# Kernel optimization log

Measured on AMD Instinct MI355X. Metric: run time of the kernel, lower is better.

Reference implementation:

```python
import jax, jax.numpy as jnp
import numpy as np

V, E, H = 2048, 512, 1024  # vocab, emb_dim, hid_dim
B, L = 128, 256            # batch, seq_len


def _gru_cell(x, h, W_ih, W_hh, b_ih, b_hh):
    # PyTorch GRU cell math. x: [B, in], h: [B, H]
    gi = x @ W_ih.T + b_ih            # [B, 3H]
    gh = h @ W_hh.T + b_hh            # [B, 3H]
    i_r, i_z, i_n = jnp.split(gi, 3, axis=-1)
    h_r, h_z, h_n = jnp.split(gh, 3, axis=-1)
    r = jax.nn.sigmoid(i_r + h_r)
    z = jax.nn.sigmoid(i_z + h_z)
    n = jnp.tanh(i_n + r * h_n)
    return (1.0 - z) * n + z * h


def setup_inputs() -> dict:
    key = jax.random.key(0)
    ks = jax.random.split(key, 16)
    s = 0.05
    emb_enc = jax.random.normal(ks[0], (V, E), jnp.float32) * s
    emb_dec = jax.random.normal(ks[1], (V, E), jnp.float32) * s
    # padding_idx=0 rows are zero in nn.Embedding
    emb_enc = emb_enc.at[0].set(0.0)
    emb_dec = emb_dec.at[0].set(0.0)
    inp = {
        "seq": jax.random.randint(ks[2], (B, L), 0, V, jnp.int64 if jax.config.jax_enable_x64 else jnp.int32),
        "teacher_forcing_ratio": 1,
        "emb_enc": emb_enc,
        "W_ih_e": jax.random.normal(ks[3], (3 * H, E), jnp.float32) * s,
        "W_hh_e": jax.random.normal(ks[4], (3 * H, H), jnp.float32) * s,
        "b_ih_e": jax.random.normal(ks[5], (3 * H,), jnp.float32) * s,
        "b_hh_e": jax.random.normal(ks[6], (3 * H,), jnp.float32) * s,
        "emb_dec": emb_dec,
        "W_ih_d": jax.random.normal(ks[7], (3 * H, E + H), jnp.float32) * s,
        "W_hh_d": jax.random.normal(ks[8], (3 * H, H), jnp.float32) * s,
        "b_ih_d": jax.random.normal(ks[9], (3 * H,), jnp.float32) * s,
        "b_hh_d": jax.random.normal(ks[10], (3 * H,), jnp.float32) * s,
        "fc_W": jax.random.normal(ks[11], (V, E + 2 * H), jnp.float32) * s,
        "fc_b": jax.random.normal(ks[12], (V,), jnp.float32) * s,
    }
    return inp


def reference(seq, teacher_forcing_ratio, emb_enc, W_ih_e, W_hh_e, b_ih_e, b_hh_e,
              emb_dec, W_ih_d, W_hh_d, b_ih_d, b_hh_d, fc_W, fc_b):
    # ---- Encoder: GRU over embedded seq (dropout_p=0, eval mode) ----
    x_emb = emb_enc[seq]                       # [B, L, E]
    h0 = jnp.zeros((seq.shape[0], H), x_emb.dtype)

    def enc_step(h, x_t):
        return _gru_cell(x_t, h, W_ih_e, W_hh_e, b_ih_e, b_hh_e), None

    context, _ = jax.lax.scan(enc_step, h0, jnp.swapaxes(x_emb, 0, 1))  # [B, H]
    mu = jnp.zeros((seq.shape[0], H), jnp.float32)
    log_var = jnp.zeros((seq.shape[0], H), jnp.float32)

    # ---- Decoder: teacher_forcing_ratio=1 -> inputs are seq[:, t-1] for step t ----
    dec_in = emb_dec[seq[:, :-1]]              # [B, L-1, E]

    def dec_step(h, e_t):
        x = jnp.concatenate([e_t, context], axis=-1)            # [B, E+H]
        h2 = _gru_cell(x, h, W_ih_d, W_hh_d, b_ih_d, b_hh_d)    # [B, H]
        feat = jnp.concatenate([e_t, h2, context], axis=-1)     # [B, E+2H]
        pred = feat @ fc_W.T + fc_b                             # [B, V]
        return h2, pred

    _, preds = jax.lax.scan(dec_step, context, jnp.swapaxes(dec_in, 0, 1))  # [L-1, B, V]
    preds = jnp.swapaxes(preds, 0, 1)                                        # [B, L-1, V]
    outputs = jnp.concatenate(
        [jnp.zeros((seq.shape[0], 1, V), preds.dtype), preds], axis=1)      # [B, L, V]
    return outputs, context, mu, log_var
```

## Files before the change

### kernel.cpp

```cpp
#include <hip/hip_runtime.h>
#include <math.h>

#define KV 2048
#define KE 512
#define KH 1024
#define KB 128
#define KL 256
#define KH3 3072
#define TCH 32
#define NSLOT 33

typedef __attribute__((ext_vector_type(8))) short s8v;
typedef __attribute__((ext_vector_type(8))) unsigned short u16x8;
typedef __attribute__((ext_vector_type(4))) float f4v;

__device__ __forceinline__ unsigned short f2b(float f) {
    unsigned u = __float_as_uint(f);
    u += 0x7fffu + ((u >> 16) & 1u);
    return (unsigned short)(u >> 16);
}
__device__ __forceinline__ float b2f(unsigned short h) {
    return __uint_as_float(((unsigned)h) << 16);
}

template<int ROWS>
__device__ __forceinline__ void stage_tile(unsigned short* lds,
                                           const unsigned short* g, int ld)
{
    const int tid = threadIdx.x;
    const int wave = tid >> 6, lane = tid & 63;
    constexpr int per_wave = ROWS / 32;
    #pragma unroll
    for (int i = 0; i < per_wave; ++i) {
        const int r0 = (wave * per_wave + i) * 8;
        const int r  = r0 + (lane >> 3);
        const int cg = (lane & 7) ^ (r & 7);
        const unsigned short* gp = g + (size_t)r * ld + cg * 8;
        __builtin_amdgcn_global_load_lds(
            (const __attribute__((address_space(1))) unsigned int*)(const void*)gp,
            (__attribute__((address_space(3))) unsigned int*)(void*)(lds + r0 * 64),
            16, 0, 0);
    }
}

__global__ __launch_bounds__(256)
void gemm128(const unsigned short* __restrict__ A, int lda,
             const unsigned short* __restrict__ Bm, int ldb,
             float* __restrict__ OutF, unsigned short* __restrict__ OutH,
             int N, int K,
             const float* __restrict__ bias,
             const float* __restrict__ addrow,
             int scatter, int t0)
{
    __shared__ unsigned short As[128 * 64];
    __shared__ unsigned short Bs[128 * 64];
    const int tid = threadIdx.x;
    const int wave = tid >> 6, lane = tid & 63;
    const int wm = wave >> 1, wn = wave & 1;
    const int q = lane >> 4, l15 = lane & 15, l7 = lane & 7;
    const int m0 = blockIdx.y * 128, n0 = blockIdx.x * 128;
    f4v acc[4][4] = {};
    for (int kb = 0; kb < K; kb += 64) {
        stage_tile<128>(As, A + (size_t)m0 * lda + kb, lda);
        stage_tile<128>(Bs, Bm + (size_t)n0 * ldb + kb, ldb);
        __syncthreads();
        #pragma unroll
        for (int kk = 0; kk < 2; ++kk) {
            const int ch = (kk * 4 + q) ^ l7;
            s8v a[4], b[4];
            #pragma unroll
            for (int i = 0; i < 4; ++i) {
                a[i] = *(const s8v*)(As + (wm * 64 + i * 16 + l15) * 64 + ch * 8);
                b[i] = *(const s8v*)(Bs + (wn * 64 + i * 16 + l15) * 64 + ch * 8);
            }
            #pragma unroll
            for (int i = 0; i < 4; ++i)
                #pragma unroll
                for (int j = 0; j < 4; ++j)
                    acc[i][j] = __builtin_amdgcn_mfma_f32_16x16x32_bf16(
                        a[i], b[j], acc[i][j], 0, 0, 0);
        }
        __syncthreads();
    }
    #pragma unroll
    for (int i = 0; i < 4; ++i) {
        #pragma unroll
        for (int r = 0; r < 4; ++r) {
            const int row = m0 + wm * 64 + i * 16 + q * 4 + r;
            size_t obase;
            if (scatter) {
                const int bidx = row & 127, tl = row >> 7;
                obase = (size_t)(bidx * KL + t0 + tl + 1) * KV;
            } else {
                obase = (size_t)row * N;
            }
            #pragma unroll
            for (int j = 0; j < 4; ++j) {
                const int col = n0 + wn * 64 + j * 16 + l15;
                float v = acc[i][j][r];
                if (bias)   v += bias[col];
                if (addrow) v += addrow[(size_t)(row & 127) * N + col];
                if (OutF) OutF[obase + col] = v;
                else      OutH[obase + col] = f2b(v);
            }
        }
    }
}

__global__ __launch_bounds__(256)
void rec_fused(const unsigned short* __restrict__ gi,
               const float* __restrict__ ci,
               unsigned short* hbring,
               float* __restrict__ h,
               unsigned short* __restrict__ h2,
               const unsigned short* __restrict__ Whh,
               const float* __restrict__ bhh,
               unsigned* bar, int Tc, unsigned gen0, int slot0)
{
    __shared__ unsigned short Ws[3 * 16 * KH];
    __shared__ float Pp[4 * 6 * 4 * 16 * 4];
    __shared__ unsigned short Hs[32 * 16];
    unsigned* flags = bar + 64;
    const int tid  = threadIdx.x;
    const int wave = tid >> 6, lane = tid & 63;
    const int q = lane >> 4, l15 = lane & 15;
    const int mg  = (int)blockIdx.x & 3;
    const int m0  = mg * 32;
    const int hc0 = ((int)blockIdx.x >> 2) * 16;

    #pragma unroll
    for (int it = 0; it < 24; ++it) {
        const int gidx = it * 256 + tid;
        const int row  = gidx >> 7;
        const int slot = gidx & 127;
        const int csrc = slot ^ (row & 7);
        const int g = row >> 4, rr = row & 15;
        const unsigned short* src =
            Whh + (size_t)(g * KH + hc0 + rr) * KH + csrc * 8;
        __builtin_amdgcn_global_load_lds(
            (const __attribute__((address_space(1))) unsigned int*)(const void*)src,
            (__attribute__((address_space(3))) unsigned int*)(void*)(Ws + row * KH + slot * 8),
            16, 0, 0);
    }

    const int col16 = tid & 15;
    const int rowq  = (tid >> 4) & 15;
    const int qq = rowq >> 2, r4 = rowq & 3;
    const int col = hc0 + col16;
    float bh[3], civ[2][3], hv[2];
    #pragma unroll
    for (int g = 0; g < 3; ++g) bh[g] = bhh[g * KH + col];
    #pragma unroll
    for (int i = 0; i < 2; ++i) {
        const int row = m0 + i * 16 + rowq;
        hv[i] = h[(size_t)row * KH + col];
        #pragma unroll
        for (int g = 0; g < 3; ++g)
            civ[i][g] = ci ? ci[(size_t)row * KH3 + g * KH + col] : 0.0f;
    }
    __syncthreads();

    const unsigned* fp = flags + mg * 64 + lane;

    for (int tl = 0; tl < Tc; ++tl) {
        int sl = slot0 + tl;       if (sl >= NSLOT) sl -= NSLOT;
        int slw = sl + 1;          if (slw >= NSLOT) slw -= NSLOT;
        const unsigned short* hin  = hbring + (size_t)sl  * KB * KH;
        unsigned short*       hout = hbring + (size_t)slw * KB * KH;

        float gir[2][3];
        #pragma unroll
        for (int i = 0; i < 2; ++i) {
            const size_t gib = ((size_t)tl * KB + m0 + i * 16 + rowq) * KH3 + col;
            gir[i][0] = b2f(gi[gib]);
            gir[i][1] = b2f(gi[gib + KH]);
            gir[i][2] = b2f(gi[gib + 2 * KH]);
        }

        if (tl > 0) {
            const unsigned tgt = gen0 + (unsigned)tl;
            while (true) {
                unsigned v;
                asm volatile("global_load_dword %0, %1, off sc0 sc1\n\t"
                             "s_waitcnt vmcnt(0)"
                             : "=v"(v) : "v"(fp) : "memory");
                if (!__any((int)(v < tgt))) break;
                __builtin_amdgcn_s_sleep(1);
            }
        }

        s8v a[2][8];
        #pragma unroll
        for (int i = 0; i < 2; ++i)
            #pragma unroll
            for (int kk = 0; kk < 8; ++kk)
                a[i][kk] = *(const s8v*)(hin +
                    (size_t)(m0 + i * 16 + l15) * KH + wave * 256 + kk * 32 + q * 8);

        f4v acc[2][3] = {};
        #pragma unroll
        for (int kk = 0; kk < 8; ++kk) {
            const int soff = ((wave * 32 + kk * 4 + q) ^ (l15 & 7)) * 8;
            #pragma unroll
            for (int g = 0; g < 3; ++g) {
                const s8v bf = *(const s8v*)(Ws + (g * 16 + l15) * KH + soff);
                acc[0][g] = __builtin_amdgcn_mfma_f32_16x16x32_bf16(
                    a[0][kk], bf, acc[0][g], 0, 0, 0);
                acc[1][g] = __builtin_amdgcn_mfma_f32_16x16x32_bf16(
                    a[1][kk], bf, acc[1][g], 0, 0, 0);
            }
        }
        #pragma unroll
        for (int i = 0; i < 2; ++i)
            #pragma unroll
            for (int g = 0; g < 3; ++g)
                *(f4v*)(Pp + (((wave * 6 + i * 3 + g) * 4 + q) * 16 + l15) * 4)
                    = acc[i][g];
        __syncthreads();
        #pragma unroll
        for (int i = 0; i < 2; ++i) {
            float gs0 = 0.f, gs1 = 0.f, gs2 = 0.f;
            #pragma unroll
            for (int w = 0; w < 4; ++w) {
                const float* p = Pp + ((w * 6 + i * 3) * 4 + qq) * 64
                               + col16 * 4 + r4;
                gs0 += p[0]; gs1 += p[256]; gs2 += p[512];
            }
            const float rg = 1.0f / (1.0f + __expf(-(gir[i][0] + civ[i][0] + gs0 + bh[0])));
            const float zg = 1.0f / (1.0f + __expf(-(gir[i][1] + civ[i][1] + gs1 + bh[1])));
            const float ng = tanhf(gir[i][2] + civ[i][2] + rg * (gs2 + bh[2]));
            hv[i] = (1.0f - zg) * ng + zg * hv[i];
            const unsigned short hb16 = f2b(hv[i]);
            const int li = i * 16 + rowq;
            Hs[li * 16 + col16] = hb16;
            if (h2) h2[((size_t)tl * KB + m0 + li) * (KE + KH) + col] = hb16;
        }
        __syncthreads();
        if (wave == 0) {
            const int row = lane >> 1, half = lane & 1;
            const u16x8 hval = *(const u16x8*)(Hs + row * 16 + half * 8);
            const unsigned short* sp =
                hout + (size_t)(m0 + row) * KH + hc0 + half * 8;
            asm volatile("global_store_dwordx4 %0, %1, off sc0 sc1"
                         :: "v"(sp), "v"(hval) : "memory");
            asm volatile("s_waitcnt vmcnt(0)" ::: "memory");
            if (lane == 0) {
                const unsigned tgt = gen0 + (unsigned)tl + 1u;
                const unsigned* fpw = flags + mg * 64 + ((int)blockIdx.x >> 2);
                asm volatile("global_store_dword %0, %1, off sc0 sc1"
                             :: "v"(fpw), "v"(tgt) : "memory");
            }
        }
    }
    #pragma unroll
    for (int i = 0; i < 2; ++i)
        h[(size_t)(m0 + i * 16 + rowq) * KH + col] = hv[i];
}

static void launch_rec(const unsigned short* gi, const float* ci,
                       unsigned short* hbring, float* h, unsigned short* h2,
                       const unsigned short* Whh, const float* bhh,
                       unsigned* bar, int Tc, unsigned gen0, int slot0,
                       hipStream_t stream)
{
    void* args[11] = { (void*)&gi, (void*)&ci, (void*)&hbring, (void*)&h,
                       (void*)&h2, (void*)&Whh, (void*)&bhh, (void*)&bar,
                       (void*)&Tc, (void*)&gen0, (void*)&slot0 };
    hipLaunchCooperativeKernel((const void*)rec_fused, dim3(256), dim3(256),
                               args, 0, stream);
}

__global__ __launch_bounds__(256)
void gather_emb(const float* __restrict__ emb, const int* __restrict__ seq,
                unsigned short* __restrict__ X, int ldx, int t0)
{
    const int idx = blockIdx.x * 256 + threadIdx.x;
    const int e8 = idx & 63;
    const int rr = idx >> 6;
    const int b = rr & 127, tl = rr >> 7;
    const int tok = seq[b * KL + t0 + tl];
    const float4* src = (const float4*)(emb + (size_t)tok * KE + e8 * 8);
    const float4 v0 = src[0], v1 = src[1];
    u16x8 o;
    o[0] = f2b(v0.x); o[1] = f2b(v0.y); o[2] = f2b(v0.z); o[3] = f2b(v0.w);
    o[4] = f2b(v1.x); o[5] = f2b(v1.y); o[6] = f2b(v1.z); o[7] = f2b(v1.w);
    *(u16x8*)(X + (size_t)rr * ldx + e8 * 8) = o;
}

__global__ __launch_bounds__(256)
void f32tobf16(const float* __restrict__ src, unsigned short* __restrict__ dst, int n)
{
    const int i = (blockIdx.x * 256 + threadIdx.x) * 4;
    if (i < n) {
        const float4 v = *(const float4*)(src + i);
        dst[i] = f2b(v.x); dst[i + 1] = f2b(v.y);
        dst[i + 2] = f2b(v.z); dst[i + 3] = f2b(v.w);
    }
}

__global__ __launch_bounds__(256)
void zero_f32(float* __restrict__ p, int n)
{
    const int i = blockIdx.x * 256 + threadIdx.x;
    if (i < n) p[i] = 0.0f;
}

__global__ __launch_bounds__(256)
void zero_u16(unsigned short* __restrict__ p, int n)
{
    const int i = blockIdx.x * 256 + threadIdx.x;
    if (i < n) p[i] = 0;
}

__global__ __launch_bounds__(256)
void copy_f32(float* __restrict__ dst, const float* __restrict__ src, int n)
{
    const int i = blockIdx.x * 256 + threadIdx.x;
    if (i < n) dst[i] = src[i];
}

__global__ __launch_bounds__(256)
void zero_row0(float* __restrict__ out)
{
    const int idx = blockIdx.x * 256 + threadIdx.x;
    const int b = idx >> 11, v = idx & (KV - 1);
    out[(size_t)b * KL * KV + v] = 0.0f;
}

extern "C" void kernel_launch(void* const* d_in, const int* in_sizes, int n_in,
                              void* d_out, int out_size, void* d_ws, size_t ws_size,
                              hipStream_t stream)
{
    (void)in_sizes; (void)n_in; (void)out_size; (void)ws_size;
    const int*   seq     = (const int*)  d_in[0];
    const float* emb_enc = (const float*)d_in[2];
    const float* W_ih_e  = (const float*)d_in[3];
    const float* W_hh_e  = (const float*)d_in[4];
    const float* b_ih_e  = (const float*)d_in[5];
    const float* b_hh_e  = (const float*)d_in[6];
    const float* emb_dec = (const float*)d_in[7];
    const float* W_ih_d  = (const float*)d_in[8];
    const float* W_hh_d  = (const float*)d_in[9];
    const float* b_ih_d  = (const float*)d_in[10];
    const float* b_hh_d  = (const float*)d_in[11];
    const float* fc_W    = (const float*)d_in[12];
    const float* fc_b    = (const float*)d_in[13];
    float* out = (float*)d_out;

    char* w = (char*)d_ws;
    unsigned*       bar     = (unsigned*)w;                  w += 2048;
    unsigned short* Wb_ih_e = (unsigned short*)w;            w += (size_t)KH3 * KE * 2;
    unsigned short* Wb_hh_e = (unsigned short*)w;            w += (size_t)KH3 * KH * 2;
    unsigned short* Wb_ih_d = (unsigned short*)w;            w += (size_t)KH3 * (KE + KH) * 2;
    unsigned short* Wb_hh_d = (unsigned short*)w;            w += (size_t)KH3 * KH * 2;
    unsigned short* fc_Wb   = (unsigned short*)w;            w += (size_t)KV * (KE + 2 * KH) * 2;
    float*          h       = (float*)w;                     w += (size_t)KB * KH * 4;
    unsigned short* hbring  = (unsigned short*)w;            w += (size_t)NSLOT * KB * KH * 2;
    float*          ci      = (float*)w;                     w += (size_t)KB * KH3 * 4;
    float*          cf      = (float*)w;                     w += (size_t)KB * KV * 4;
    unsigned short* gi      = (unsigned short*)w;            w += (size_t)TCH * KB * KH3 * 2;
    unsigned short* featc   = (unsigned short*)w;            w += (size_t)TCH * KB * (KE + KH) * 2;

    f32tobf16<<<(KH3 * KE) / 1024, 256, 0, stream>>>(W_ih_e, Wb_ih_e, KH3 * KE);
    f32tobf16<<<(KH3 * KH) / 1024, 256, 0, stream>>>(W_hh_e, Wb_hh_e, KH3 * KH);
    f32tobf16<<<(KH3 * (KE + KH)) / 1024, 256, 0, stream>>>(W_ih_d, Wb_ih_d, KH3 * (KE + KH));
    f32tobf16<<<(KH3 * KH) / 1024, 256, 0, stream>>>(W_hh_d, Wb_hh_d, KH3 * KH);
    f32tobf16<<<(KV * (KE + 2 * KH)) / 1024, 256, 0, stream>>>(fc_W, fc_Wb, KV * (KE + 2 * KH));

    zero_f32<<<2, 256, 0, stream>>>((float*)bar, 512);
    zero_f32<<<(KB * KH) / 256, 256, 0, stream>>>(h, KB * KH);
    zero_u16<<<(KB * KH) / 256, 256, 0, stream>>>(hbring, KB * KH);

    unsigned gen0 = 0;
    int slot = 0;

    for (int t0 = 0; t0 < KL; t0 += TCH) {
        unsigned short* Xc = featc;
        gather_emb<<<(TCH * KB * 64) / 256, 256, 0, stream>>>(emb_enc, seq, Xc, KE, t0);
        gemm128<<<dim3(KH3 / 128, (TCH * KB) / 128), 256, 0, stream>>>(
            Xc, KE, Wb_ih_e, KE, nullptr, gi, KH3, KE, b_ih_e, nullptr, 0, 0);
        launch_rec(gi, nullptr, hbring, h, nullptr, Wb_hh_e, b_hh_e, bar,
                   TCH, gen0, slot, stream);
        gen0 += TCH;
        slot = (slot + TCH) % NSLOT;
    }

    const unsigned short* ctxb = hbring + (size_t)slot * KB * KH;

    float* ctx_out = out + (size_t)KB * KL * KV;
    copy_f32<<<(KB * KH) / 256, 256, 0, stream>>>(ctx_out, h, KB * KH);
    zero_f32<<<(2 * KB * KH) / 256, 256, 0, stream>>>(ctx_out + KB * KH, 2 * KB * KH);
    zero_row0<<<(KB * KV) / 256, 256, 0, stream>>>(out);

    gemm128<<<dim3(KH3 / 128, 1), 256, 0, stream>>>(
        ctxb, KH, Wb_ih_d + KE, KE + KH, ci, nullptr, KH3, KH, b_ih_d, nullptr, 0, 0);
    gemm128<<<dim3(KV / 128, 1), 256, 0, stream>>>(
        ctxb, KH, fc_Wb + (KE + KH), KE + 2 * KH, cf, nullptr, KV, KH, fc_b, nullptr, 0, 0);

    for (int t0 = 0; t0 < KL - 1; t0 += TCH) {
        const int Tc = ((KL - 1 - t0) < TCH) ? (KL - 1 - t0) : TCH;
        gather_emb<<<(Tc * KB * 64) / 256, 256, 0, stream>>>(emb_dec, seq, featc, KE + KH, t0);
        gemm128<<<dim3(KH3 / 128, (Tc * KB) / 128), 256, 0, stream>>>(
            featc, KE + KH, Wb_ih_d, KE + KH, nullptr, gi, KH3, KE, nullptr, nullptr, 0, 0);
        launch_rec(gi, ci, hbring, h, featc + KE, Wb_hh_d, b_hh_d, bar,
                   Tc, gen0, slot, stream);
        gen0 += Tc;
        slot = (slot + Tc) % NSLOT;
        gemm128<<<dim3(KV / 128, (Tc * KB) / 128), 256, 0, stream>>>(
            featc, KE + KH, fc_Wb, KE + 2 * KH, out, nullptr, KV, KE + KH,
            nullptr, cf, 1, t0);
    }
}
```

Baseline: 4.724 ms.

## Replace per-block flag array with atomic counter barrier and direct packed h stores

Each block now has every thread compute two adjacent hidden columns and store them as a packed dword straight to the global ring buffer. This removes the LDS staging buffer and the single-wave store step. Per-block flag words polled with a wave-wide any are replaced by one atomic counter per row group, which pollers compare against 64 times the generation. The intent is to shorten the per-step critical path of the recurrent barrier. It relies on the counter layout and initialisation matching the new 64x target scheme, and it adds atomic contention from 64 blocks per counter.

After: 4.268 ms. -9.6%, faster.

```diff
diff --git a/kernel.cpp b/kernel.cpp
--- a/kernel.cpp
+++ b/kernel.cpp
@@ -119,14 +119,13 @@
 {
     __shared__ unsigned short Ws[3 * 16 * KH];
     __shared__ float Pp[4 * 6 * 4 * 16 * 4];
-    __shared__ unsigned short Hs[32 * 16];
-    unsigned* flags = bar + 64;
     const int tid  = threadIdx.x;
     const int wave = tid >> 6, lane = tid & 63;
     const int q = lane >> 4, l15 = lane & 15;
     const int mg  = (int)blockIdx.x & 3;
     const int m0  = mg * 32;
     const int hc0 = ((int)blockIdx.x >> 2) * 16;
+    unsigned* cnt = bar + mg * 64;
 
     #pragma unroll
     for (int it = 0; it < 24; ++it) {
@@ -143,24 +142,27 @@
             16, 0, 0);
     }
 
-    const int col16 = tid & 15;
-    const int rowq  = (tid >> 4) & 15;
-    const int qq = rowq >> 2, r4 = rowq & 3;
-    const int col = hc0 + col16;
-    float bh[3], civ[2][3], hv[2];
+    const int erow = tid >> 3;
+    const int cp   = (tid & 7) * 2;
+    const int i_   = erow >> 4;
+    const int qq   = (erow >> 2) & 3;
+    const int r4   = erow & 3;
+    const int grow = m0 + erow;
+    const int gcol = hc0 + cp;
+    float bh0[3], bh1[3], civ0[3], civ1[3];
+    float hv0, hv1;
     #pragma unroll
-    for (int g = 0; g < 3; ++g) bh[g] = bhh[g * KH + col];
-    #pragma unroll
-    for (int i = 0; i < 2; ++i) {
-        const int row = m0 + i * 16 + rowq;
-        hv[i] = h[(size_t)row * KH + col];
-        #pragma unroll
-        for (int g = 0; g < 3; ++g)
-            civ[i][g] = ci ? ci[(size_t)row * KH3 + g * KH + col] : 0.0f;
-    }
+    for (int g = 0; g < 3; ++g) {
+        bh0[g] = bhh[g * KH + gcol];
+        bh1[g] = bhh[g * KH + gcol + 1];
+        if (ci) {
+            civ0[g] = ci[(size_t)grow * KH3 + g * KH + gcol];
+            civ1[g] = ci[(size_t)grow * KH3 + g * KH + gcol + 1];
+        } else { civ0[g] = 0.0f; civ1[g] = 0.0f; }
+    }
+    hv0 = h[(size_t)grow * KH + gcol];
+    hv1 = h[(size_t)grow * KH + gcol + 1];
     __syncthreads();
-
-    const unsigned* fp = flags + mg * 64 + lane;
 
     for (int tl = 0; tl < Tc; ++tl) {
         int sl = slot0 + tl;       if (sl >= NSLOT) sl -= NSLOT;
@@ -168,23 +170,20 @@
         const unsigned short* hin  = hbring + (size_t)sl  * KB * KH;
         unsigned short*       hout = hbring + (size_t)slw * KB * KH;
 
-        float gir[2][3];
-        #pragma unroll
-        for (int i = 0; i < 2; ++i) {
-            const size_t gib = ((size_t)tl * KB + m0 + i * 16 + rowq) * KH3 + col;
-            gir[i][0] = b2f(gi[gib]);
-            gir[i][1] = b2f(gi[gib + KH]);
-            gir[i][2] = b2f(gi[gib + 2 * KH]);
-        }
+        unsigned giw[3];
+        #pragma unroll
+        for (int g = 0; g < 3; ++g)
+            giw[g] = *(const unsigned*)(gi +
+                ((size_t)tl * KB + grow) * KH3 + g * KH + gcol);
 
         if (tl > 0) {
-            const unsigned tgt = gen0 + (unsigned)tl;
+            const unsigned tgt = 64u * (gen0 + (unsigned)tl);
             while (true) {
                 unsigned v;
                 asm volatile("global_load_dword %0, %1, off sc0 sc1\n\t"
                              "s_waitcnt vmcnt(0)"
-                             : "=v"(v) : "v"(fp) : "memory");
-                if (!__any((int)(v < tgt))) break;
+                             : "=v"(v) : "v"(cnt) : "memory");
+                if (v >= tgt) break;
                 __builtin_amdgcn_s_sleep(1);
             }
         }
@@ -217,44 +216,41 @@
                 *(f4v*)(Pp + (((wave * 6 + i * 3 + g) * 4 + q) * 16 + l15) * 4)
                     = acc[i][g];
         __syncthreads();
-        #pragma unroll
-        for (int i = 0; i < 2; ++i) {
-            float gs0 = 0.f, gs1 = 0.f, gs2 = 0.f;
-            #pragma unroll
-            for (int w = 0; w < 4; ++w) {
-                const float* p = Pp + ((w * 6 + i * 3) * 4 + qq) * 64
-                               + col16 * 4 + r4;
-                gs0 += p[0]; gs1 += p[256]; gs2 += p[512];
-            }
-            const float rg = 1.0f / (1.0f + __expf(-(gir[i][0] + civ[i][0] + gs0 + bh[0])));
-            const float zg = 1.0f / (1.0f + __expf(-(gir[i][1] + civ[i][1] + gs1 + bh[1])));
-            const float ng = tanhf(gir[i][2] + civ[i][2] + rg * (gs2 + bh[2]));
-            hv[i] = (1.0f - zg) * ng + zg * hv[i];
-            const unsigned short hb16 = f2b(hv[i]);
-            const int li = i * 16 + rowq;
-            Hs[li * 16 + col16] = hb16;
-            if (h2) h2[((size_t)tl * KB + m0 + li) * (KE + KH) + col] = hb16;
-        }
+
+        float gs0[3], gs1[3];
+        #pragma unroll
+        for (int g = 0; g < 3; ++g) { gs0[g] = 0.f; gs1[g] = 0.f; }
+        #pragma unroll
+        for (int w = 0; w < 4; ++w)
+            #pragma unroll
+            for (int g = 0; g < 3; ++g) {
+                const float* p = Pp + ((w * 6 + i_ * 3 + g) * 4 + qq) * 64 + r4;
+                gs0[g] += p[cp * 4];
+                gs1[g] += p[cp * 4 + 4];
+            }
+        const float rg0 = 1.0f / (1.0f + __expf(-(b2f((unsigned short)(giw[0] & 0xffff)) + civ0[0] + gs0[0] + bh0[0])));
+        const float zg0 = 1.0f / (1.0f + __expf(-(b2f((unsigned short)(giw[1] & 0xffff)) + civ0[1] + gs0[1] + bh0[1])));
+        const float ng0 = tanhf(b2f((unsigned short)(giw[2] & 0xffff)) + civ0[2] + rg0 * (gs0[2] + bh0[2]));
+        hv0 = (1.0f - zg0) * ng0 + zg0 * hv0;
+        const float rg1 = 1.0f / (1.0f + __expf(-(b2f((unsigned short)(giw[0] >> 16)) + civ1[0] + gs1[0] + bh1[0])));
+        const float zg1 = 1.0f / (1.0f + __expf(-(b2f((unsigned short)(giw[1] >> 16)) + civ1[1] + gs1[1] + bh1[1])));
+        const float ng1 = tanhf(b2f((unsigned short)(giw[2] >> 16)) + civ1[2] + rg1 * (gs1[2] + bh1[2]));
+        hv1 = (1.0f - zg1) * ng1 + zg1 * hv1;
+
+        const unsigned hpack = (unsigned)f2b(hv0) | ((unsigned)f2b(hv1) << 16);
+        const unsigned short* sp = hout + (size_t)grow * KH + gcol;
+        asm volatile("global_store_dword %0, %1, off sc0 sc1"
+                     :: "v"(sp), "v"(hpack) : "memory");
+        if (h2)
+            *(unsigned*)(h2 + ((size_t)tl * KB + grow) * (KE + KH) + gcol) = hpack;
+
+        asm volatile("s_waitcnt vmcnt(0)" ::: "memory");
         __syncthreads();
-        if (wave == 0) {
-            const int row = lane >> 1, half = lane & 1;
-            const u16x8 hval = *(const u16x8*)(Hs + row * 16 + half * 8);
-            const unsigned short* sp =
-                hout + (size_t)(m0 + row) * KH + hc0 + half * 8;
-            asm volatile("global_store_dwordx4 %0, %1, off sc0 sc1"
-                         :: "v"(sp), "v"(hval) : "memory");
-            asm volatile("s_waitcnt vmcnt(0)" ::: "memory");
-            if (lane == 0) {
-                const unsigned tgt = gen0 + (unsigned)tl + 1u;
-                const unsigned* fpw = flags + mg * 64 + ((int)blockIdx.x >> 2);
-                asm volatile("global_store_dword %0, %1, off sc0 sc1"
-                             :: "v"(fpw), "v"(tgt) : "memory");
-            }
-        }
-    }
-    #pragma unroll
-    for (int i = 0; i < 2; ++i)
-        h[(size_t)(m0 + i * 16 + rowq) * KH + col] = hv[i];
+        if (tid == 0)
+            __hip_atomic_fetch_add(cnt, 1u, __ATOMIC_RELAXED,
+                                   __HIP_MEMORY_SCOPE_AGENT);
+    }
+    *(float2*)(h + (size_t)grow * KH + gcol) = make_float2(hv0, hv1);
 }
 
 static void launch_rec(const unsigned short* gi, const float* ci,
```
